# Kernel tuning notes

Hardware: AMD Instinct MI355X
Metric: run time of the kernel (lower is better)

Reference implementation:

```python
import jax, jax.numpy as jnp
import numpy as np

S, N, NSUB, F, HID, NH = 8, 20000, 4000, 128, 64, 8


def setup_inputs() -> dict:
    key = jax.random.key(0)
    ks = jax.random.split(key, 24)
    # unique sorted node indices per snapshot (matches snap.nodes used for gather + scatter-pad)
    nodes = jnp.stack([jnp.sort(jax.random.permutation(ks[i], N)[:NSUB]) for i in range(S)])
    # dense normalized adjacency proxy (norm_adj.to_dense()); scaled so rows sum ~1
    adj = jax.random.uniform(ks[8], (S, NSUB, NSUB), dtype=jnp.float32) * (2.0 / NSUB)
    p = lambda k, shp: jax.random.normal(k, shp, dtype=jnp.float32) * 0.02
    return {
        "nodes": nodes,
        "adj": adj,
        "emb": p(ks[9], (N, F)),
        "W1": p(ks[10], (F, HID)), "b1": jnp.zeros((HID,), jnp.float32),
        "W2": p(ks[11], (HID, HID)), "b2": jnp.zeros((HID,), jnp.float32),
        "time_emb": p(ks[12], (2 * S - 1, NH)),
        "Wq": p(ks[13], (HID, HID)), "bq": jnp.zeros((HID,), jnp.float32),
        "Wk": p(ks[14], (HID, HID)), "bk": jnp.zeros((HID,), jnp.float32),
        "Wv": p(ks[15], (HID, HID)), "bv": jnp.zeros((HID,), jnp.float32),
        "Wo": p(ks[16], (HID, HID)), "bo": jnp.zeros((HID,), jnp.float32),
    }


def reference(nodes, adj, emb, W1, b1, W2, b2, time_emb,
              Wq, bq, Wk, bk, Wv, bv, Wo, bo):
    s, nsub = nodes.shape
    n_total, _ = emb.shape
    hid = W1.shape[1]
    nh = time_emb.shape[1]
    dh = hid // nh
    # per-snapshot GCN encode (2 layers of A @ (X W) + b, ReLU), vectorized over snapshots
    feat = emb[nodes]                                            # [S, n, F]
    h = jax.nn.relu(jnp.einsum('sij,sjh->sih', adj, feat @ W1) + b1)
    h = jax.nn.relu(jnp.einsum('sij,sjh->sih', adj, h @ W2) + b2)
    # scatter-pad into zero buffer of size nodes_num (output[pos_idx] = x)
    x = jnp.zeros((s, n_total, hid), h.dtype).at[jnp.arange(s)[:, None], nodes].set(h)
    x = x.transpose(1, 0, 2)                                     # [N, S, HID]
    # relative-position time bias: Embedding(2S-1, NH)[rel_matrix] -> [NH, S, S]
    rel = jnp.arange(s)[None, :] - jnp.arange(s)[:, None] + s - 1
    bias = time_emb[rel].transpose(2, 0, 1)
    # multi-head attention over the snapshot axis, batch = nodes
    q = (x @ Wq + bq).reshape(n_total, s, nh, dh) * (dh ** -0.5)
    k = (x @ Wk + bk).reshape(n_total, s, nh, dh)
    v = (x @ Wv + bv).reshape(n_total, s, nh, dh)
    scores = jnp.einsum('nqhd,nkhd->nhqk', q, k) + bias          # [N, NH, S, S]
    attn = jax.nn.softmax(scores, axis=-1)
    o = jnp.einsum('nhqk,nkhd->nqhd', attn, v).reshape(n_total, s, hid)
    o = o @ Wo + bo
    o = o.transpose(1, 0, 2)                                     # [S, N, HID]
    # gather active nodes back, then structure decoder z @ z.T per snapshot
    z = jnp.take_along_axis(o, nodes[:, :, None], axis=1)        # [S, n, HID]
    out = jnp.einsum('sid,sjd->sij', z, z)                       # [S, n, n]
    return out
```

## Files before the change

### kernel.cpp

```cpp
#include <hip/hip_runtime.h>
#include <hip/hip_bf16.h>
#include <cstdint>

#define S 8
#define NTOT 20000
#define NSUB 4000
#define NSUBP 4032
#define NST 63
#define F 128
#define HID 64
#define NH 8
#define DH 8

typedef __attribute__((ext_vector_type(8))) short bf16x8;
typedef __attribute__((ext_vector_type(4))) short bf16x4;
typedef __attribute__((ext_vector_type(4))) float f32x4;

__device__ __forceinline__ short f2bf(float f) {
  union { __hip_bfloat16 h; short s; } u;
  u.h = __float2bfloat16(f);
  return u.s;
}

__device__ __forceinline__ void gload16(const void* gsrc, void* ldst) {
  __builtin_amdgcn_global_load_lds(
      (const __attribute__((address_space(1))) void*)gsrc,
      (__attribute__((address_space(3))) void*)ldst, 16, 0, 0);
}

__global__ void k_pos_init(int* __restrict__ posIdx) {
  int t = blockIdx.x * 256 + threadIdx.x;
  if (t < NTOT * S) posIdx[t] = -1;
}

__global__ void k_pos_scatter(const int* __restrict__ nodes, int* __restrict__ posIdx) {
  int t = blockIdx.x * 256 + threadIdx.x;
  if (t < S * NSUB) {
    int s = t / NSUB, i = t - s * NSUB;
    posIdx[nodes[t] * S + s] = i;
  }
}

__global__ void k_pt_pad(short* __restrict__ Pt) {
  int t = blockIdx.x * 256 + threadIdx.x;
  int seg = t >> 2, off = (t & 3) * 8;
  bf16x8 z = (bf16x8){0,0,0,0,0,0,0,0};
  *(bf16x8*)(Pt + (size_t)seg * NSUBP + NSUB + off) = z;
}

__global__ void k_w2t(const float* __restrict__ W2, short* __restrict__ W2t) {
  int t = blockIdx.x * 256 + threadIdx.x;
  int j = t >> 6, k = t & 63;
  W2t[t] = f2bf(W2[k * HID + j]);
}

__global__ __launch_bounds__(256) void k_feat_w1(const int* __restrict__ nodes,
                                                 const float* __restrict__ emb,
                                                 const float* __restrict__ W1,
                                                 short* __restrict__ Pt) {
  __shared__ __align__(16) float feat[16][F];
  __shared__ float tr[64][17];
  int t = threadIdx.x;
  int s = blockIdx.x / 250;
  int i0 = (blockIdx.x - s * 250) * 16;
  int gr0 = blockIdx.x * 16;
  int lr = t >> 4, lc = (t & 15) * 8;
  int n = nodes[gr0 + lr];
  *(f32x4*)&feat[lr][lc]     = *(const f32x4*)(emb + (size_t)n * F + lc);
  *(f32x4*)&feat[lr][lc + 4] = *(const f32x4*)(emb + (size_t)n * F + lc + 4);
  __syncthreads();
  int j = t & 63, ig = t >> 6;
  float acc[4] = {0.f, 0.f, 0.f, 0.f};
  for (int k = 0; k < F; ++k) {
    float w = W1[k * HID + j];
    #pragma unroll
    for (int i = 0; i < 4; ++i) acc[i] += feat[ig * 4 + i][k] * w;
  }
  #pragma unroll
  for (int i = 0; i < 4; ++i) tr[j][ig * 4 + i] = acc[i];
  __syncthreads();
  int jr = t >> 2, seg = (t & 3) * 4;
  bf16x4 o;
  #pragma unroll
  for (int u = 0; u < 4; ++u) o[u] = f2bf(tr[jr][seg + u]);
  *(bf16x4*)(Pt + ((size_t)s * HID + jr) * NSUBP + i0 + seg) = o;
}

template<int MODE>
__global__ __launch_bounds__(256) void k_adj(const float* __restrict__ adj,
                                             const short* __restrict__ Pt,
                                             const float* __restrict__ bias,
                                             const short* __restrict__ W2t,
                                             float* __restrict__ outF,
                                             short* __restrict__ outB) {
  __shared__ __align__(16) float As[2][64 * 64];
  __shared__ __align__(16) short Bs[2][64 * 64];
  __shared__ __align__(16) short hb[MODE == 0 ? 4 * 16 * 64 : 4];
  __shared__ __align__(16) short tb[MODE == 0 ? 4 * 64 * 24 : 4];
  int bid = blockIdx.x;
  int s = bid & 7;
  int mb = bid >> 3;
  int tid = threadIdx.x;
  int w = tid >> 6, lane = tid & 63, l15 = lane & 15, g = lane >> 4;
  int m0 = mb * 64;
  const float* adjS = adj + (size_t)s * NSUB * NSUB;
  const short* PtS  = Pt  + (size_t)s * HID * NSUBP;

  int rbase = w * 4 + (lane >> 4);
  int sigA = l15;
  int clogA = (sigA & 8) | ((sigA & 7) ^ (rbase & 7));
  int acolf = clogA * 4;
  const float* arow[4];
  #pragma unroll
  for (int p = 0; p < 4; ++p) {
    int rg = m0 + p * 16 + rbase;
    rg = rg < NSUB ? rg : NSUB - 1;
    arow[p] = adjS + (size_t)rg * NSUB;
  }
  int sigB = lane & 7;
  int clogB = sigB ^ ((lane >> 3) & 7);
  const short* bsrc[2];
  #pragma unroll
  for (int p = 0; p < 2; ++p) {
    int col = p * 32 + w * 8 + (lane >> 3);
    bsrc[p] = PtS + (size_t)col * NSUBP + clogB * 8;
  }

  char* As0 = (char*)&As[0][0];
  char* Bs0 = (char*)&Bs[0][0];
  int wb = w * 1024;

  int arowf = w * 16 + l15;
  int aoff = arowf * 256 + (((2 * g) ^ (arowf & 7)) * 16);
  int boff[4];
  #pragma unroll
  for (int nf = 0; nf < 4; ++nf) {
    int col = nf * 16 + l15;
    boff[nf] = col * 128 + ((g ^ (col & 7)) * 16);
  }

  f32x4 acc[4];
  #pragma unroll
  for (int nf = 0; nf < 4; ++nf) acc[nf] = (f32x4){0.f, 0.f, 0.f, 0.f};

  #pragma unroll
  for (int p = 0; p < 4; ++p)
    gload16(arow[p] + acolf, As0 + p * 4096 + wb);
  #pragma unroll
  for (int p = 0; p < 2; ++p)
    gload16(bsrc[p], Bs0 + p * 4096 + wb);

  for (int t = 0; t < NST; ++t) {
    __syncthreads();
    int cur = t & 1;
    if (t + 1 < NST) {
      int kn = (t + 1) * 64;
      bool ok = (kn + acolf) < NSUB;
      char* nA = As0 + (cur ^ 1) * 16384;
      char* nB = Bs0 + (cur ^ 1) * 8192;
      #pragma unroll
      for (int p = 0; p < 4; ++p)
        gload16(ok ? (arow[p] + kn + acolf) : arow[p], nA + p * 4096 + wb);
      #pragma unroll
      for (int p = 0; p < 2; ++p)
        gload16(bsrc[p] + kn, nB + p * 4096 + wb);
    }
    const char* Ab = As0 + cur * 16384;
    const char* Bb = Bs0 + cur * 8192;
    f32x4 a0 = *(const f32x4*)(Ab + aoff);
    f32x4 a1 = *(const f32x4*)(Ab + (aoff ^ 16));
    f32x4 a2 = *(const f32x4*)(Ab + 128 + aoff);
    f32x4 a3 = *(const f32x4*)(Ab + 128 + (aoff ^ 16));
    bf16x8 af0, af1;
    af0[0] = f2bf(a0.x); af0[1] = f2bf(a0.y); af0[2] = f2bf(a0.z); af0[3] = f2bf(a0.w);
    af0[4] = f2bf(a1.x); af0[5] = f2bf(a1.y); af0[6] = f2bf(a1.z); af0[7] = f2bf(a1.w);
    af1[0] = f2bf(a2.x); af1[1] = f2bf(a2.y); af1[2] = f2bf(a2.z); af1[3] = f2bf(a2.w);
    af1[4] = f2bf(a3.x); af1[5] = f2bf(a3.y); af1[6] = f2bf(a3.z); af1[7] = f2bf(a3.w);
    #pragma unroll
    for (int nf = 0; nf < 4; ++nf) {
      bf16x8 b0 = *(const bf16x8*)(Bb + boff[nf]);
      bf16x8 b1 = *(const bf16x8*)(Bb + (boff[nf] ^ 64));
      acc[nf] = __builtin_amdgcn_mfma_f32_16x16x32_bf16(af0, b0, acc[nf], 0, 0, 0);
      acc[nf] = __builtin_amdgcn_mfma_f32_16x16x32_bf16(af1, b1, acc[nf], 0, 0, 0);
    }
  }

  if constexpr (MODE == 1) {
    float* P = outF + (size_t)s * NSUB * HID;
    #pragma unroll
    for (int nf = 0; nf < 4; ++nf) {
      int col = nf * 16 + l15;
      float bv = bias[col];
      #pragma unroll
      for (int r = 0; r < 4; ++r) {
        int row = m0 + w * 16 + g * 4 + r;
        if (row < NSUB) P[(size_t)row * HID + col] = fmaxf(acc[nf][r] + bv, 0.f);
      }
    }
  } else {
    char* hbw = (char*)&hb[0] + w * 2048;
    #pragma unroll
    for (int nf = 0; nf < 4; ++nf) {
      int col = nf * 16 + l15;
      float bv = bias[col];
      #pragma unroll
      for (int r = 0; r < 4; ++r) {
        int r16 = g * 4 + r;
        float hv = fmaxf(acc[nf][r] + bv, 0.f);
        int byte = r16 * 128 + (((col >> 3) ^ (r16 & 7)) * 16) + (col & 7) * 2;
        *(short*)(hbw + byte) = f2bf(hv);
      }
    }
    __syncthreads();
    short* tbw = &tb[0] + w * 1536;
    #pragma unroll
    for (int jf = 0; jf < 4; ++jf) {
      f32x4 o = (f32x4){0.f, 0.f, 0.f, 0.f};
      #pragma unroll
      for (int kk = 0; kk < 2; ++kk) {
        bf16x8 a = *(const bf16x8*)(hbw + l15 * 128 + (((kk * 4 + g) ^ (l15 & 7)) * 16));
        bf16x8 b = *(const bf16x8*)(W2t + (jf * 16 + l15) * HID + kk * 32 + g * 8);
        o = __builtin_amdgcn_mfma_f32_16x16x32_bf16(a, b, o, 0, 0, 0);
      }
      #pragma unroll
      for (int r = 0; r < 4; ++r)
        tbw[(jf * 16 + l15) * 24 + g * 4 + r] = f2bf(o[r]);
    }
    __syncthreads();
    int j = tid >> 2, wv = tid & 3;
    #pragma unroll
    for (int c = 0; c < 2; ++c) {
      int gi = m0 + wv * 16 + c * 8;
      bf16x8 v = *(const bf16x8*)(&tb[0] + wv * 1536 + j * 24 + c * 8);
      if (gi >= NSUB) v = (bf16x8){0,0,0,0,0,0,0,0};
      *(bf16x8*)(outB + ((size_t)s * HID + j) * NSUBP + gi) = v;
    }
  }
}

__global__ __launch_bounds__(256) void k_attn(const float* __restrict__ H,
                                              const int* __restrict__ posIdx,
                                              const float* __restrict__ Wq, const float* __restrict__ bq,
                                              const float* __restrict__ Wk, const float* __restrict__ bk,
                                              const float* __restrict__ Wv, const float* __restrict__ bv,
                                              const float* __restrict__ Wo, const float* __restrict__ bo,
                                              const float* __restrict__ te,
                                              short* __restrict__ Zb) {
  __shared__ __align__(16) float xk[4][S][HID];
  __shared__ __align__(16) float qs[4][S][HID];
  __shared__ __align__(16) float ks[4][S][HID];
  __shared__ __align__(16) float vs[4][S][HID];
  __shared__ __align__(16) float os[4][S][HID];
  int w = threadIdx.x >> 6;
  int lane = threadIdx.x & 63;
  int n = blockIdx.x * 4 + w;
  int pi[S];
  #pragma unroll
  for (int s = 0; s < S; ++s) {
    pi[s] = posIdx[n * S + s];
    xk[w][s][lane] = (pi[s] >= 0) ? H[((size_t)s * NSUB + pi[s]) * HID + lane] : 0.f;
  }
  __syncthreads();
  float aq[S], ak[S], av[S];
  #pragma unroll
  for (int s = 0; s < S; ++s) { aq[s] = bq[lane]; ak[s] = bk[lane]; av[s] = bv[lane]; }
  for (int k = 0; k < HID; ++k) {
    float wq = Wq[k*HID + lane], wk_ = Wk[k*HID + lane], wv = Wv[k*HID + lane];
    #pragma unroll
    for (int s = 0; s < S; ++s) {
      float xv = xk[w][s][k];
      aq[s] += xv * wq; ak[s] += xv * wk_; av[s] += xv * wv;
    }
  }
  const float qscale = 0.35355339059327373f;
  #pragma unroll
  for (int s = 0; s < S; ++s) {
    qs[w][s][lane] = aq[s] * qscale;
    ks[w][s][lane] = ak[s];
    vs[w][s][lane] = av[s];
  }
  __syncthreads();
  int h = lane >> 3, sq = lane & 7;
  f32x4 q0 = *(const f32x4*)&qs[w][sq][h * DH];
  f32x4 q1 = *(const f32x4*)&qs[w][sq][h * DH + 4];
  float sc[S];
  #pragma unroll
  for (int t = 0; t < S; ++t) {
    f32x4 k0v = *(const f32x4*)&ks[w][t][h * DH];
    f32x4 k1v = *(const f32x4*)&ks[w][t][h * DH + 4];
    float d = q0.x*k0v.x + q0.y*k0v.y + q0.z*k0v.z + q0.w*k0v.w
            + q1.x*k1v.x + q1.y*k1v.y + q1.z*k1v.z + q1.w*k1v.w;
    sc[t] = d + te[(t - sq + S - 1) * NH + h];
  }
  float m = sc[0];
  #pragma unroll
  for (int t = 1; t < S; ++t) m = fmaxf(m, sc[t]);
  float sum = 0.f;
  #pragma unroll
  for (int t = 0; t < S; ++t) { sc[t] = expf(sc[t] - m); sum += sc[t]; }
  float inv = 1.f / sum;
  f32x4 o0 = (f32x4){0.f,0.f,0.f,0.f}, o1 = (f32x4){0.f,0.f,0.f,0.f};
  #pragma unroll
  for (int t = 0; t < S; ++t) {
    f32x4 v0 = *(const f32x4*)&vs[w][t][h * DH];
    f32x4 v1 = *(const f32x4*)&vs[w][t][h * DH + 4];
    #pragma unroll
    for (int u = 0; u < 4; ++u) { o0[u] += sc[t] * v0[u]; o1[u] += sc[t] * v1[u]; }
  }
  #pragma unroll
  for (int u = 0; u < 4; ++u) { o0[u] *= inv; o1[u] *= inv; }
  *(f32x4*)&os[w][sq][h * DH]     = o0;
  *(f32x4*)&os[w][sq][h * DH + 4] = o1;
  __syncthreads();
  float ao[S];
  #pragma unroll
  for (int s = 0; s < S; ++s) ao[s] = bo[lane];
  for (int k = 0; k < HID; ++k) {
    float wo = Wo[k*HID + lane];
    #pragma unroll
    for (int s = 0; s < S; ++s) ao[s] += os[w][s][k] * wo;
  }
  #pragma unroll
  for (int s = 0; s < S; ++s)
    if (pi[s] >= 0) Zb[((size_t)s * NSUB + pi[s]) * HID + lane] = f2bf(ao[s]);
}

__global__ __launch_bounds__(256) void k_dec(const short* __restrict__ Zb,
                                             float* __restrict__ out) {
  __shared__ __align__(16) float tr[4][16][68];
  int bid = blockIdx.x;
  int s = bid & 7;
  int tt = bid >> 3;
  int by = tt / 63, bx = tt - by * 63;
  int wave = threadIdx.x >> 6, lane = threadIdx.x & 63;
  int l15 = lane & 15, g = lane >> 4;
  int m0 = by * 64 + wave * 16;
  int n0 = bx * 64;
  const short* ZS = Zb + (size_t)s * NSUB * HID;
  int mrow = m0 + l15;
  int mc = mrow < NSUB ? mrow : NSUB - 1;
  bf16x8 a0 = *(const bf16x8*)(ZS + (size_t)mc * HID + g * 8);
  bf16x8 a1 = *(const bf16x8*)(ZS + (size_t)mc * HID + 32 + g * 8);
  f32x4 acc[4];
  #pragma unroll
  for (int nf = 0; nf < 4; ++nf) acc[nf] = (f32x4){0.f, 0.f, 0.f, 0.f};
  #pragma unroll
  for (int nf = 0; nf < 4; ++nf) {
    int ncol = n0 + nf * 16 + l15;
    int nc = ncol < NSUB ? ncol : NSUB - 1;
    bf16x8 b0 = *(const bf16x8*)(ZS + (size_t)nc * HID + g * 8);
    bf16x8 b1 = *(const bf16x8*)(ZS + (size_t)nc * HID + 32 + g * 8);
    acc[nf] = __builtin_amdgcn_mfma_f32_16x16x32_bf16(a0, b0, acc[nf], 0, 0, 0);
    acc[nf] = __builtin_amdgcn_mfma_f32_16x16x32_bf16(a1, b1, acc[nf], 0, 0, 0);
  }
  #pragma unroll
  for (int nf = 0; nf < 4; ++nf)
    #pragma unroll
    for (int r = 0; r < 4; ++r)
      tr[wave][g * 4 + r][nf * 16 + l15] = acc[nf][r];
  __syncthreads();
  float* outS = out + (size_t)s * NSUB * NSUB;
  #pragma unroll
  for (int p = 0; p < 4; ++p) {
    int rr = p * 4 + g;
    int grow = m0 + rr;
    int gcol = n0 + l15 * 4;
    f32x4 v = *(const f32x4*)&tr[wave][rr][l15 * 4];
    if (grow < NSUB && gcol < NSUB)
      __builtin_nontemporal_store(v, (f32x4*)(outS + (size_t)grow * NSUB + gcol));
  }
}

extern "C" void kernel_launch(void* const* d_in, const int* in_sizes, int n_in,
                              void* d_out, int out_size, void* d_ws, size_t ws_size,
                              hipStream_t stream) {
  const int*   nodes = (const int*)d_in[0];
  const float* adj   = (const float*)d_in[1];
  const float* emb   = (const float*)d_in[2];
  const float* W1    = (const float*)d_in[3];
  const float* b1    = (const float*)d_in[4];
  const float* W2    = (const float*)d_in[5];
  const float* b2    = (const float*)d_in[6];
  const float* te    = (const float*)d_in[7];
  const float* Wq    = (const float*)d_in[8];
  const float* bq    = (const float*)d_in[9];
  const float* Wk    = (const float*)d_in[10];
  const float* bk    = (const float*)d_in[11];
  const float* Wv    = (const float*)d_in[12];
  const float* bv    = (const float*)d_in[13];
  const float* Wo    = (const float*)d_in[14];
  const float* bo    = (const float*)d_in[15];
  float* outp = (float*)d_out;

  float* H    = (float*)d_ws;
  short* Pt1  = (short*)(H + (size_t)S * NSUB * HID);
  short* Pt2  = Pt1 + (size_t)S * HID * NSUBP;
  short* Zb   = Pt2 + (size_t)S * HID * NSUBP;
  int* posIdx = (int*)(Zb + (size_t)S * NSUB * HID);
  short* W2t  = (short*)(posIdx + (size_t)NTOT * S);

  k_pos_init<<<(NTOT*S + 255)/256, 256, 0, stream>>>(posIdx);
  k_pos_scatter<<<(S*NSUB + 255)/256, 256, 0, stream>>>(nodes, posIdx);
  k_pt_pad<<<8, 256, 0, stream>>>(Pt1);
  k_w2t<<<16, 256, 0, stream>>>(W2, W2t);

  k_feat_w1<<<2000, 256, 0, stream>>>(nodes, emb, W1, Pt1);
  k_adj<0><<<504, 256, 0, stream>>>(adj, Pt1, b1, W2t, nullptr, Pt2);
  k_adj<1><<<504, 256, 0, stream>>>(adj, Pt2, b2, nullptr, H, nullptr);
  k_attn<<<NTOT/4, 256, 0, stream>>>(H, posIdx, Wq, bq, Wk, bk, Wv, bv, Wo, bo, te, Zb);
  k_dec<<<63*63*8, 256, 0, stream>>>(Zb, outp);
}
```

Baseline: 472.1 us.

## Use bf16 MFMA for attention QKV and output projections

Replaces the scalar fp32 FMA loops for the Q/K/V and output projections in the attention kernel with 16x16x32 bf16 MFMA instructions. Input activations and attention outputs are staged as bf16 in XOR-swizzled LDS tiles. A new preprocessing kernel transposes the four projection weights to bf16. This cuts ALU and weight-load cost but wastes half the MFMA rows, since S=8 is padded to 16, and lowers projection precision to bf16.

```diff
diff --git a/kernel.cpp b/kernel.cpp
--- a/kernel.cpp
+++ b/kernel.cpp
@@ -52,6 +52,16 @@
   int t = blockIdx.x * 256 + threadIdx.x;
   int j = t >> 6, k = t & 63;
   W2t[t] = f2bf(W2[k * HID + j]);
+}
+
+__global__ void k_wt(const float* __restrict__ Wq, const float* __restrict__ Wk,
+                     const float* __restrict__ Wv, const float* __restrict__ Wo,
+                     short* __restrict__ Wt) {
+  int t = blockIdx.x * 256 + threadIdx.x;
+  int p = t >> 12, rem = t & 4095;
+  int j = rem >> 6, k = rem & 63;
+  const float* src = (p == 0) ? Wq : (p == 1) ? Wk : (p == 2) ? Wv : Wo;
+  Wt[t] = f2bf(src[k * HID + j]);
 }
 
 __global__ __launch_bounds__(256) void k_feat_w1(const int* __restrict__ nodes,
@@ -240,44 +250,58 @@
 
 __global__ __launch_bounds__(256) void k_attn(const float* __restrict__ H,
                                               const int* __restrict__ posIdx,
-                                              const float* __restrict__ Wq, const float* __restrict__ bq,
-                                              const float* __restrict__ Wk, const float* __restrict__ bk,
-                                              const float* __restrict__ Wv, const float* __restrict__ bv,
-                                              const float* __restrict__ Wo, const float* __restrict__ bo,
+                                              const short* __restrict__ Wt,
+                                              const float* __restrict__ bq,
+                                              const float* __restrict__ bk,
+                                              const float* __restrict__ bv,
+                                              const float* __restrict__ bo,
                                               const float* __restrict__ te,
                                               short* __restrict__ Zb) {
-  __shared__ __align__(16) float xk[4][S][HID];
+  __shared__ __align__(16) short xb[4 * 16 * 64];
+  __shared__ __align__(16) short ob[4 * 16 * 64];
   __shared__ __align__(16) float qs[4][S][HID];
   __shared__ __align__(16) float ks[4][S][HID];
   __shared__ __align__(16) float vs[4][S][HID];
-  __shared__ __align__(16) float os[4][S][HID];
   int w = threadIdx.x >> 6;
   int lane = threadIdx.x & 63;
+  int l15 = lane & 15, g = lane >> 4;
   int n = blockIdx.x * 4 + w;
+  char* xbw = (char*)xb + w * 2048;
+  char* obw = (char*)ob + w * 2048;
   int pi[S];
   #pragma unroll
   for (int s = 0; s < S; ++s) {
     pi[s] = posIdx[n * S + s];
-    xk[w][s][lane] = (pi[s] >= 0) ? H[((size_t)s * NSUB + pi[s]) * HID + lane] : 0.f;
-  }
-  __syncthreads();
-  float aq[S], ak[S], av[S];
-  #pragma unroll
-  for (int s = 0; s < S; ++s) { aq[s] = bq[lane]; ak[s] = bk[lane]; av[s] = bv[lane]; }
-  for (int k = 0; k < HID; ++k) {
-    float wq = Wq[k*HID + lane], wk_ = Wk[k*HID + lane], wv = Wv[k*HID + lane];
-    #pragma unroll
-    for (int s = 0; s < S; ++s) {
-      float xv = xk[w][s][k];
-      aq[s] += xv * wq; ak[s] += xv * wk_; av[s] += xv * wv;
-    }
-  }
+    float xv = (pi[s] >= 0) ? H[((size_t)s * NSUB + pi[s]) * HID + lane] : 0.f;
+    *(short*)(xbw + s * 128 + (((lane >> 3) ^ s) * 16) + (lane & 7) * 2) = f2bf(xv);
+  }
+  __syncthreads();
   const float qscale = 0.35355339059327373f;
   #pragma unroll
-  for (int s = 0; s < S; ++s) {
-    qs[w][s][lane] = aq[s] * qscale;
-    ks[w][s][lane] = ak[s];
-    vs[w][s][lane] = av[s];
+  for (int p = 0; p < 3; ++p) {
+    const short* W = Wt + p * 4096;
+    #pragma unroll
+    for (int nf = 0; nf < 4; ++nf) {
+      int col = nf * 16 + l15;
+      f32x4 o = (f32x4){0.f, 0.f, 0.f, 0.f};
+      #pragma unroll
+      for (int kk = 0; kk < 2; ++kk) {
+        bf16x8 a = *(const bf16x8*)(xbw + l15 * 128 + (((kk * 4 + g) ^ (l15 & 7)) * 16));
+        bf16x8 b = *(const bf16x8*)(W + col * HID + kk * 32 + g * 8);
+        o = __builtin_amdgcn_mfma_f32_16x16x32_bf16(a, b, o, 0, 0, 0);
+      }
+      float bia = (p == 0) ? bq[col] : (p == 1) ? bk[col] : bv[col];
+      #pragma unroll
+      for (int r = 0; r < 4; ++r) {
+        int s = g * 4 + r;
+        if (s < S) {
+          float v = o[r] + bia;
+          if (p == 0) qs[w][s][col] = v * qscale;
+          else if (p == 1) ks[w][s][col] = v;
+          else vs[w][s][col] = v;
+        }
+      }
+    }
   }
   __syncthreads();
   int h = lane >> 3, sq = lane & 7;
@@ -307,22 +331,30 @@
     #pragma unroll
     for (int u = 0; u < 4; ++u) { o0[u] += sc[t] * v0[u]; o1[u] += sc[t] * v1[u]; }
   }
-  #pragma unroll
-  for (int u = 0; u < 4; ++u) { o0[u] *= inv; o1[u] *= inv; }
-  *(f32x4*)&os[w][sq][h * DH]     = o0;
-  *(f32x4*)&os[w][sq][h * DH + 4] = o1;
-  __syncthreads();
-  float ao[S];
-  #pragma unroll
-  for (int s = 0; s < S; ++s) ao[s] = bo[lane];
-  for (int k = 0; k < HID; ++k) {
-    float wo = Wo[k*HID + lane];
-    #pragma unroll
-    for (int s = 0; s < S; ++s) ao[s] += os[w][s][k] * wo;
-  }
-  #pragma unroll
-  for (int s = 0; s < S; ++s)
-    if (pi[s] >= 0) Zb[((size_t)s * NSUB + pi[s]) * HID + lane] = f2bf(ao[s]);
+  bf16x8 ov;
+  #pragma unroll
+  for (int u = 0; u < 4; ++u) { ov[u] = f2bf(o0[u] * inv); ov[u + 4] = f2bf(o1[u] * inv); }
+  *(bf16x8*)(obw + sq * 128 + ((h ^ sq) * 16)) = ov;
+  __syncthreads();
+  const short* Wo_ = Wt + 3 * 4096;
+  #pragma unroll
+  for (int nf = 0; nf < 4; ++nf) {
+    int col = nf * 16 + l15;
+    f32x4 o = (f32x4){0.f, 0.f, 0.f, 0.f};
+    #pragma unroll
+    for (int kk = 0; kk < 2; ++kk) {
+      bf16x8 a = *(const bf16x8*)(obw + l15 * 128 + (((kk * 4 + g) ^ (l15 & 7)) * 16));
+      bf16x8 b = *(const bf16x8*)(Wo_ + col * HID + kk * 32 + g * 8);
+      o = __builtin_amdgcn_mfma_f32_16x16x32_bf16(a, b, o, 0, 0, 0);
+    }
+    float bia = bo[col];
+    #pragma unroll
+    for (int r = 0; r < 4; ++r) {
+      int s = g * 4 + r;
+      if (s < S && pi[s] >= 0)
+        Zb[((size_t)s * NSUB + pi[s]) * HID + col] = f2bf(o[r] + bia);
+    }
+  }
 }
 
 __global__ __launch_bounds__(256) void k_dec(const short* __restrict__ Zb,
@@ -398,15 +430,17 @@
   short* Zb   = Pt2 + (size_t)S * HID * NSUBP;
   int* posIdx = (int*)(Zb + (size_t)S * NSUB * HID);
   short* W2t  = (short*)(posIdx + (size_t)NTOT * S);
+  short* Wt   = W2t + 64 * 64;
 
   k_pos_init<<<(NTOT*S + 255)/256, 256, 0, stream>>>(posIdx);
   k_pos_scatter<<<(S*NSUB + 255)/256, 256, 0, stream>>>(nodes, posIdx);
   k_pt_pad<<<8, 256, 0, stream>>>(Pt1);
   k_w2t<<<16, 256, 0, stream>>>(W2, W2t);
+  k_wt<<<64, 256, 0, stream>>>(Wq, Wk, Wv, Wo, Wt);
 
   k_feat_w1<<<2000, 256, 0, stream>>>(nodes, emb, W1, Pt1);
   k_adj<0><<<504, 256, 0, stream>>>(adj, Pt1, b1, W2t, nullptr, Pt2);
   k_adj<1><<<504, 256, 0, stream>>>(adj, Pt2, b2, nullptr, H, nullptr);
-  k_attn<<<NTOT/4, 256, 0, stream>>>(H, posIdx, Wq, bq, Wk, bk, Wv, bv, Wo, bo, te, Zb);
+  k_attn<<<NTOT/4, 256, 0, stream>>>(H, posIdx, Wt, bq, bk, bv, bo, te, Zb);
   k_dec<<<63*63*8, 256, 0, stream>>>(Zb, outp);
 }
```

Result: no change. 476.2 us (+0.9%).

## Pre-convert adjacency to tiled bf16 once and share across both GCN passes

Applied to the files above, without the earlier changes.

Adds a conversion kernel that reads the fp32 adjacency once and writes a bf16 copy laid out as swizzled 64x64 tiles per row stripe. Both adjacency GEMM passes then stream half the bytes per pass with contiguous tile loads and no in-loop fp32-to-bf16 conversion. This costs an extra full fp32 read plus a bf16 write, and a large workspace buffer.

```diff
diff --git a/kernel.cpp b/kernel.cpp
--- a/kernel.cpp
+++ b/kernel.cpp
@@ -52,6 +52,41 @@
   int t = blockIdx.x * 256 + threadIdx.x;
   int j = t >> 6, k = t & 63;
   W2t[t] = f2bf(W2[k * HID + j]);
+}
+
+__global__ __launch_bounds__(256) void k_conv(const float* __restrict__ adj,
+                                              short* __restrict__ adjb) {
+  int bid = blockIdx.x;
+  int s = bid & 7;
+  int half = (bid >> 3) & 1;
+  int mb = bid >> 4;
+  int w = threadIdx.x >> 6, lane = threadIdx.x & 63;
+  const float* adjS = adj + (size_t)s * NSUB * NSUB;
+  short* stripe = adjb + (size_t)(s * 63 + mb) * 63 * 4096;
+  int ktl = lane >> 3;
+  int c = lane & 7;
+  for (int rr = 0; rr < 8; ++rr) {
+    int r = half * 32 + w * 8 + rr;
+    int mr = mb * 64 + r; if (mr >= NSUB) mr = NSUB - 1;
+    const float* rowp = adjS + (size_t)mr * NSUB;
+    #pragma unroll
+    for (int it = 0; it < 8; ++it) {
+      int kt = it * 8 + ktl;
+      if (kt < 63) {
+        int k0 = kt * 64 + c * 8;
+        bf16x8 o;
+        if (k0 < NSUB) {
+          f32x4 v0 = __builtin_nontemporal_load((const f32x4*)(rowp + k0));
+          f32x4 v1 = __builtin_nontemporal_load((const f32x4*)(rowp + k0 + 4));
+          o[0]=f2bf(v0.x); o[1]=f2bf(v0.y); o[2]=f2bf(v0.z); o[3]=f2bf(v0.w);
+          o[4]=f2bf(v1.x); o[5]=f2bf(v1.y); o[6]=f2bf(v1.z); o[7]=f2bf(v1.w);
+        } else {
+          o = (bf16x8){0,0,0,0,0,0,0,0};
+        }
+        *(bf16x8*)(stripe + (size_t)kt * 4096 + r * 64 + ((c ^ (r & 7)) * 8)) = o;
+      }
+    }
+  }
 }
 
 __global__ __launch_bounds__(256) void k_feat_w1(const int* __restrict__ nodes,
@@ -87,13 +122,13 @@
 }
 
 template<int MODE>
-__global__ __launch_bounds__(256) void k_adj(const float* __restrict__ adj,
+__global__ __launch_bounds__(256) void k_adj(const short* __restrict__ adjb,
                                              const short* __restrict__ Pt,
                                              const float* __restrict__ bias,
                                              const short* __restrict__ W2t,
                                              float* __restrict__ outF,
                                              short* __restrict__ outB) {
-  __shared__ __align__(16) float As[2][64 * 64];
+  __shared__ __align__(16) short As[2][64 * 64];
   __shared__ __align__(16) short Bs[2][64 * 64];
   __shared__ __align__(16) short hb[MODE == 0 ? 4 * 16 * 64 : 4];
   __shared__ __align__(16) short tb[MODE == 0 ? 4 * 64 * 24 : 4];
@@ -103,22 +138,11 @@
   int tid = threadIdx.x;
   int w = tid >> 6, lane = tid & 63, l15 = lane & 15, g = lane >> 4;
   int m0 = mb * 64;
-  const float* adjS = adj + (size_t)s * NSUB * NSUB;
-  const short* PtS  = Pt  + (size_t)s * HID * NSUBP;
-
-  int rbase = w * 4 + (lane >> 4);
-  int sigA = l15;
-  int clogA = (sigA & 8) | ((sigA & 7) ^ (rbase & 7));
-  int acolf = clogA * 4;
-  const float* arow[4];
-  #pragma unroll
-  for (int p = 0; p < 4; ++p) {
-    int rg = m0 + p * 16 + rbase;
-    rg = rg < NSUB ? rg : NSUB - 1;
-    arow[p] = adjS + (size_t)rg * NSUB;
-  }
-  int sigB = lane & 7;
-  int clogB = sigB ^ ((lane >> 3) & 7);
+  const short* stripe = adjb + (size_t)(s * 63 + mb) * 63 * 4096;
+  const short* PtS = Pt + (size_t)s * HID * NSUBP;
+
+  int aoffS = w * 512 + lane * 8;
+  int clogB = (lane & 7) ^ ((lane >> 3) & 7);
   const short* bsrc[2];
   #pragma unroll
   for (int p = 0; p < 2; ++p) {
@@ -131,7 +155,7 @@
   int wb = w * 1024;
 
   int arowf = w * 16 + l15;
-  int aoff = arowf * 256 + (((2 * g) ^ (arowf & 7)) * 16);
+  int aoff = arowf * 128 + ((g ^ (arowf & 7)) * 16);
   int boff[4];
   #pragma unroll
   for (int nf = 0; nf < 4; ++nf) {
@@ -144,8 +168,8 @@
   for (int nf = 0; nf < 4; ++nf) acc[nf] = (f32x4){0.f, 0.f, 0.f, 0.f};
 
   #pragma unroll
-  for (int p = 0; p < 4; ++p)
-    gload16(arow[p] + acolf, As0 + p * 4096 + wb);
+  for (int p = 0; p < 2; ++p)
+    gload16(stripe + aoffS + p * 2048, As0 + p * 4096 + wb);
   #pragma unroll
   for (int p = 0; p < 2; ++p)
     gload16(bsrc[p], Bs0 + p * 4096 + wb);
@@ -154,28 +178,21 @@
     __syncthreads();
     int cur = t & 1;
     if (t + 1 < NST) {
+      const short* ntile = stripe + (size_t)(t + 1) * 4096;
       int kn = (t + 1) * 64;
-      bool ok = (kn + acolf) < NSUB;
-      char* nA = As0 + (cur ^ 1) * 16384;
+      char* nA = As0 + (cur ^ 1) * 8192;
       char* nB = Bs0 + (cur ^ 1) * 8192;
       #pragma unroll
-      for (int p = 0; p < 4; ++p)
-        gload16(ok ? (arow[p] + kn + acolf) : arow[p], nA + p * 4096 + wb);
+      for (int p = 0; p < 2; ++p)
+        gload16(ntile + aoffS + p * 2048, nA + p * 4096 + wb);
       #pragma unroll
       for (int p = 0; p < 2; ++p)
         gload16(bsrc[p] + kn, nB + p * 4096 + wb);
     }
-    const char* Ab = As0 + cur * 16384;
+    const char* Ab = As0 + cur * 8192;
     const char* Bb = Bs0 + cur * 8192;
-    f32x4 a0 = *(const f32x4*)(Ab + aoff);
-    f32x4 a1 = *(const f32x4*)(Ab + (aoff ^ 16));
-    f32x4 a2 = *(const f32x4*)(Ab + 128 + aoff);
-    f32x4 a3 = *(const f32x4*)(Ab + 128 + (aoff ^ 16));
-    bf16x8 af0, af1;
-    af0[0] = f2bf(a0.x); af0[1] = f2bf(a0.y); af0[2] = f2bf(a0.z); af0[3] = f2bf(a0.w);
-    af0[4] = f2bf(a1.x); af0[5] = f2bf(a1.y); af0[6] = f2bf(a1.z); af0[7] = f2bf(a1.w);
-    af1[0] = f2bf(a2.x); af1[1] = f2bf(a2.y); af1[2] = f2bf(a2.z); af1[3] = f2bf(a2.w);
-    af1[4] = f2bf(a3.x); af1[5] = f2bf(a3.y); af1[6] = f2bf(a3.z); af1[7] = f2bf(a3.w);
+    bf16x8 af0 = *(const bf16x8*)(Ab + aoff);
+    bf16x8 af1 = *(const bf16x8*)(Ab + (aoff ^ 64));
     #pragma unroll
     for (int nf = 0; nf < 4; ++nf) {
       bf16x8 b0 = *(const bf16x8*)(Bb + boff[nf]);
@@ -398,15 +415,17 @@
   short* Zb   = Pt2 + (size_t)S * HID * NSUBP;
   int* posIdx = (int*)(Zb + (size_t)S * NSUB * HID);
   short* W2t  = (short*)(posIdx + (size_t)NTOT * S);
+  short* adjb = W2t + 64 * 64;
 
   k_pos_init<<<(NTOT*S + 255)/256, 256, 0, stream>>>(posIdx);
   k_pos_scatter<<<(S*NSUB + 255)/256, 256, 0, stream>>>(nodes, posIdx);
   k_pt_pad<<<8, 256, 0, stream>>>(Pt1);
   k_w2t<<<16, 256, 0, stream>>>(W2, W2t);
 
+  k_conv<<<1008, 256, 0, stream>>>(adj, adjb);
   k_feat_w1<<<2000, 256, 0, stream>>>(nodes, emb, W1, Pt1);
-  k_adj<0><<<504, 256, 0, stream>>>(adj, Pt1, b1, W2t, nullptr, Pt2);
-  k_adj<1><<<504, 256, 0, stream>>>(adj, Pt2, b2, nullptr, H, nullptr);
+  k_adj<0><<<504, 256, 0, stream>>>(adjb, Pt1, b1, W2t, nullptr, Pt2);
+  k_adj<1><<<504, 256, 0, stream>>>(adjb, Pt2, b2, nullptr, H, nullptr);
   k_attn<<<NTOT/4, 256, 0, stream>>>(H, posIdx, Wq, bq, Wk, bk, Wv, bv, Wo, bo, te, Zb);
   k_dec<<<63*63*8, 256, 0, stream>>>(Zb, outp);
 }
```

Result: slower. 553.0 us (+17.2%).
